# Performance work log

Hardware: AMD Instinct MI355X
Metric: run time of the kernel (lower is better)

The kernel has to match this reference:

```python
import jax, jax.numpy as jnp
import numpy as np

N_NODES = 100000
LN_EPS = 1e-5
NEG_SLOPE = 0.2


def setup_inputs() -> dict:
    key = jax.random.key(0)
    ks = jax.random.split(key, 6)
    N, E, NIN, EDIM, NOUT, H = N_NODES, 1600000, 64, 32, 128, 4
    x = jax.random.normal(ks[0], (N, NIN), dtype=jnp.float32)
    edge_index = jax.random.randint(ks[1], (2, E), 0, N, dtype=jnp.int64)
    edge_attr = jax.random.normal(ks[2], (E, EDIM), dtype=jnp.float32)
    # xavier-uniform linear weights (torch layout: [out, in])
    def xavier(k, fan_out, fan_in):
        lim = float(np.sqrt(6.0 / (fan_in + fan_out)))
        return jax.random.uniform(k, (fan_out, fan_in), jnp.float32, -lim, lim)
    W_msg = xavier(ks[3], NOUT, NIN + EDIM)          # (128, 96)
    W_att = xavier(ks[4], H, 2 * NIN + EDIM)         # (4, 160)
    bias = jnp.zeros((NOUT,), jnp.float32)
    ln_gamma = jnp.ones((NOUT,), jnp.float32)
    ln_beta = jnp.zeros((NOUT,), jnp.float32)
    return {"x": x, "edge_index": edge_index, "edge_attr": edge_attr,
            "W_msg": W_msg, "W_att": W_att, "bias": bias,
            "ln_gamma": ln_gamma, "ln_beta": ln_beta}


def reference(x, edge_index, edge_attr, W_msg, W_att, bias, ln_gamma, ln_beta):
    N = x.shape[0]
    H = W_att.shape[0]
    src, dst = edge_index[0], edge_index[1]
    xs = x[src]                                       # (E, node_in) gather
    xd = x[dst]                                       # (E, node_in) gather
    # message: W_msg @ [h_u ; x_uv]
    msg_in = jnp.concatenate([xs, edge_attr], axis=-1)            # (E, 96)
    msgs = msg_in @ W_msg.T                                        # (E, out_dim)
    msgs = msgs.reshape(-1, H, W_msg.shape[0] // H)                # (E, H, D)
    # attention logits: LeakyReLU(W_att @ [h_u ; h_v ; x_uv])
    att_in = jnp.concatenate([xs, xd, edge_attr], axis=-1)         # (E, 160)
    logits = att_in @ W_att.T                                      # (E, H)
    logits = jax.nn.leaky_relu(logits, NEG_SLOPE)
    # per-destination-node sparse softmax
    seg_max = jax.ops.segment_max(logits, dst, num_segments=N)     # (N, H)
    exp_l = jnp.exp(logits - seg_max[dst])                         # (E, H)
    seg_sum = jax.ops.segment_sum(exp_l, dst, num_segments=N)      # (N, H)
    att = exp_l / (seg_sum[dst] + 1e-9)                            # (E, H)
    # weighted scatter-add aggregation
    weighted = msgs * att[..., None]                               # (E, H, D)
    out = jax.ops.segment_sum(weighted, dst, num_segments=N)       # (N, H, D)
    out = out.reshape(N, -1) + bias                                # concat heads
    # layer norm over feature dim
    mu = out.mean(axis=-1, keepdims=True)
    var = out.var(axis=-1, keepdims=True)
    out = (out - mu) * jax.lax.rsqrt(var + LN_EPS) * ln_gamma + ln_beta
    return out
```

## Files before the change

kernel.cpp:

```cpp
#include <hip/hip_runtime.h>
#include <hip/hip_bf16.h>

typedef __attribute__((ext_vector_type(8))) short short8;
typedef __attribute__((ext_vector_type(4))) float f32x4;

__device__ __forceinline__ unsigned short fbf(float f) {
  union { float f; unsigned u; } v; v.f = f;
  unsigned r = v.u + 0x7fffu + ((v.u >> 16) & 1u);
  return (unsigned short)(r >> 16);
}
__device__ __forceinline__ unsigned pk2(float a, float b) {
  return (unsigned)fbf(a) | ((unsigned)fbf(b) << 16);
}
__device__ __forceinline__ float ubf(unsigned hi) {
  union { unsigned u; float f; } v; v.u = hi << 16; return v.f;
}
__device__ __forceinline__ float dot4(float4 a, float4 b) {
  return fmaf(a.x, b.x, fmaf(a.y, b.y, fmaf(a.z, b.z, a.w * b.w)));
}

__global__ void k_count(const int* __restrict__ dst, int E, int* __restrict__ deg) {
  for (int i = blockIdx.x * blockDim.x + threadIdx.x; i < E; i += gridDim.x * blockDim.x)
    atomicAdd(&deg[dst[i]], 1);
}

__global__ void k_scan1(const int* __restrict__ deg, int N, int* __restrict__ part,
                        int* __restrict__ bsum) {
  __shared__ int tmp[1024];
  int tid = threadIdx.x;
  int i = blockIdx.x * 1024 + tid;
  int v = (i < N) ? deg[i] : 0;
  tmp[tid] = v;
  __syncthreads();
  for (int ofs = 1; ofs < 1024; ofs <<= 1) {
    int t = (tid >= ofs) ? tmp[tid - ofs] : 0;
    __syncthreads();
    tmp[tid] += t;
    __syncthreads();
  }
  if (i < N) part[i] = tmp[tid] - v;
  if (tid == 1023) bsum[blockIdx.x] = tmp[tid];
}

__global__ void k_scan2(int* __restrict__ part, const int* __restrict__ bsum, int N,
                        int* __restrict__ cursor) {
  __shared__ int sbase;
  if (threadIdx.x == 0) {
    int b = 0;
    for (int j = 0; j < (int)blockIdx.x; j++) b += bsum[j];
    sbase = b;
  }
  __syncthreads();
  int i = blockIdx.x * 1024 + threadIdx.x;
  if (i < N) {
    int o = part[i] + sbase;
    part[i] = o;
    cursor[i] = o;
  }
}

__global__ void k_fill(const int* __restrict__ src, const int* __restrict__ dst, int E,
                       int* __restrict__ cursor, int2* __restrict__ csr2) {
  for (int i = blockIdx.x * blockDim.x + threadIdx.x; i < E; i += gridDim.x * blockDim.x) {
    int d = dst[i];
    int slot = atomicAdd(&cursor[d], 1);
    csr2[slot] = make_int2(src[i], i);
  }
}

__launch_bounds__(256)
__global__ void k_pre(const float* __restrict__ x, const float* __restrict__ W_att,
                      float4* __restrict__ A_s, float4* __restrict__ A_d, int N) {
  __shared__ float4 s_wa[160];
  if (threadIdx.x < 160) s_wa[threadIdx.x] = ((const float4*)W_att)[threadIdx.x];
  __syncthreads();
  for (int v = blockIdx.x * blockDim.x + threadIdx.x; v < N; v += gridDim.x * blockDim.x) {
    const float4* xp = (const float4*)&x[v * 64];
    float4 xq[16];
    #pragma unroll
    for (int k = 0; k < 16; k++) xq[k] = xp[k];
    float as[4] = {}, ad[4] = {};
    #pragma unroll
    for (int h = 0; h < 4; h++) {
      #pragma unroll
      for (int k = 0; k < 16; k++) {
        as[h] += dot4(s_wa[h * 40 + k], xq[k]);
        ad[h] += dot4(s_wa[h * 40 + 16 + k], xq[k]);
      }
    }
    A_s[v] = make_float4(as[0], as[1], as[2], as[3]);
    A_d[v] = make_float4(ad[0], ad[1], ad[2], ad[3]);
  }
}

__launch_bounds__(256)
__global__ void k_cvt(const float* __restrict__ x, unsigned* __restrict__ xb2, int n4) {
  for (int i = blockIdx.x * blockDim.x + threadIdx.x; i < n4; i += gridDim.x * blockDim.x) {
    float4 t = ((const float4*)x)[i];
    xb2[i * 2]     = pk2(t.x, t.y);
    xb2[i * 2 + 1] = pk2(t.z, t.w);
  }
}

__launch_bounds__(256)
__global__ void k_agg(const unsigned short* __restrict__ xb, const float* __restrict__ ea,
                      const float4* __restrict__ A_s, const float4* __restrict__ A_d,
                      const float* __restrict__ W_att,
                      const int2* __restrict__ csr2, const int* __restrict__ offsets,
                      const int* __restrict__ deg,
                      unsigned short* __restrict__ agg, float* __restrict__ denom, int N) {
  __shared__ int2 s_ids[4][8];
  __shared__ float4 s_att[4][8];
  const int lane = threadIdx.x & 63;
  const int wvb = threadIdx.x >> 6;
  const int wv = (blockIdx.x * blockDim.x + threadIdx.x) >> 6;
  const int nw = (gridDim.x * blockDim.x) >> 6;
  const int l8 = lane & 7;
  const int l32 = lane & 31;
  const bool hi = (lane & 32) != 0;
  const int pj = lane >> 3;
  const int jc = lane & 7;

  float4 wea[4];
  #pragma unroll
  for (int h = 0; h < 4; h++)
    wea[h] = *(const float4*)&W_att[h * 160 + 128 + jc * 4];

  for (int v = wv; v < N; v += nw) {
    const int start = offsets[v];
    const int dg = deg[v];
    const float4 adv = A_d[v];
    float ax0 = 0, ax1 = 0, ax2 = 0, ax3 = 0, ae0 = 0, ae1 = 0;
    float ss0 = 0, ss1 = 0, ss2 = 0, ss3 = 0;

    if (dg > 0) {
      const int ng = (dg + 7) >> 3;
      int2 cur = csr2[start + min(l8, dg - 1)];
      for (int g = 0; g < ng; g++) {
        if (lane < 8) s_ids[wvb][lane] = cur;
        if (g + 1 < ng)
          cur = csr2[start + min((g + 1) * 8 + l8, dg - 1)];
        int2 idl = s_ids[wvb][pj];
        float4 ef = *(const float4*)&ea[(size_t)idl.y * 32 + jc * 4];
        float4 asv = A_s[idl.x];
        int sp[8], ep[8];
        #pragma unroll
        for (int p = 0; p < 8; p++) { int2 t = s_ids[wvb][p]; sp[p] = t.x; ep[p] = t.y; }
        float xv[8], ev[8];
        #pragma unroll
        for (int p = 0; p < 8; p++) xv[p] = ubf(xb[(size_t)sp[p] * 64 + lane]);
        #pragma unroll
        for (int p = 0; p < 8; p++) ev[p] = ea[(size_t)ep[p] * 32 + l32];
        float lp0 = dot4(wea[0], ef), lp1 = dot4(wea[1], ef);
        float lp2 = dot4(wea[2], ef), lp3 = dot4(wea[3], ef);
        #pragma unroll
        for (int m = 1; m <= 4; m <<= 1) {
          lp0 += __shfl_xor(lp0, m, 64);
          lp1 += __shfl_xor(lp1, m, 64);
          lp2 += __shfl_xor(lp2, m, 64);
          lp3 += __shfl_xor(lp3, m, 64);
        }
        const float msk = (g * 8 + pj < dg) ? 1.f : 0.f;
        float4 av; float lg;
        lg = lp0 + asv.x + adv.x; lg = (lg > 0.f) ? lg : 0.2f * lg; av.x = msk * __expf(lg);
        lg = lp1 + asv.y + adv.y; lg = (lg > 0.f) ? lg : 0.2f * lg; av.y = msk * __expf(lg);
        lg = lp2 + asv.z + adv.z; lg = (lg > 0.f) ? lg : 0.2f * lg; av.z = msk * __expf(lg);
        lg = lp3 + asv.w + adv.w; lg = (lg > 0.f) ? lg : 0.2f * lg; av.w = msk * __expf(lg);
        if (jc == 0) s_att[wvb][pj] = av;
        #pragma unroll
        for (int p = 0; p < 8; p++) {
          float4 ap = s_att[wvb][p];
          ax0 = fmaf(ap.x, xv[p], ax0);
          ax1 = fmaf(ap.y, xv[p], ax1);
          ax2 = fmaf(ap.z, xv[p], ax2);
          ax3 = fmaf(ap.w, xv[p], ax3);
          ae0 = fmaf(hi ? ap.z : ap.x, ev[p], ae0);
          ae1 = fmaf(hi ? ap.w : ap.y, ev[p], ae1);
          ss0 += ap.x; ss1 += ap.y; ss2 += ap.z; ss3 += ap.w;
        }
      }
    }
    const int base = v * 384;
    agg[base + lane]       = fbf(ax0);
    agg[base + 96 + lane]  = fbf(ax1);
    agg[base + 192 + lane] = fbf(ax2);
    agg[base + 288 + lane] = fbf(ax3);
    const int hA = hi ? 2 : 0;
    agg[base + hA * 96 + 64 + l32]       = fbf(ae0);
    agg[base + (hA + 1) * 96 + 64 + l32] = fbf(ae1);
    if (lane == 0) ((float4*)denom)[v] = make_float4(ss0, ss1, ss2, ss3);
  }
}

__launch_bounds__(128)
__global__ void k_out(const unsigned short* __restrict__ agg, const float* __restrict__ W_msg,
                      const float* __restrict__ denom, const float* __restrict__ bias,
                      const float* __restrict__ gamma, const float* __restrict__ beta,
                      float* __restrict__ out, int N, int T) {
  __shared__ float s_den[64];
  __shared__ float s_sum[2][16], s_sq[2][16];
  const int f = threadIdx.x;
  const int w = f >> 6;
  const int l = f & 63;
  const int c16 = l & 15;
  const int rg = l >> 4;

  short8 wb[2][2][3];
  float biasv[2][2], gv[2][2], bv[2][2];
  #pragma unroll
  for (int hh = 0; hh < 2; hh++) {
    const int head = 2 * w + hh;
    #pragma unroll
    for (int ct = 0; ct < 2; ct++) {
      const int q = head * 32 + ct * 16 + c16;
      biasv[hh][ct] = bias[q]; gv[hh][ct] = gamma[q]; bv[hh][ct] = beta[q];
      #pragma unroll
      for (int kk = 0; kk < 3; kk++) {
        const float* p = &W_msg[q * 96 + kk * 32 + rg * 8];
        short8 s;
        #pragma unroll
        for (int i = 0; i < 8; i++) s[i] = (short)fbf(p[i]);
        wb[hh][ct][kk] = s;
      }
    }
  }

  for (int t = blockIdx.x; t < T; t += gridDim.x) {
    const int n0 = t * 16;
    if (f < 64) s_den[f] = denom[min(n0 + (f >> 2), N - 1) * 4 + (f & 3)];
    __syncthreads();

    f32x4 c[2][2] = {{{0.f,0.f,0.f,0.f},{0.f,0.f,0.f,0.f}},
                     {{0.f,0.f,0.f,0.f},{0.f,0.f,0.f,0.f}}};
    const int nA = min(n0 + c16, N - 1);
    #pragma unroll
    for (int hh = 0; hh < 2; hh++) {
      const int head = 2 * w + hh;
      #pragma unroll
      for (int kk = 0; kk < 3; kk++) {
        short8 a = *(const short8*)&agg[nA * 384 + head * 96 + kk * 32 + rg * 8];
        c[hh][0] = __builtin_amdgcn_mfma_f32_16x16x32_bf16(a, wb[hh][0][kk], c[hh][0], 0, 0, 0);
        c[hh][1] = __builtin_amdgcn_mfma_f32_16x16x32_bf16(a, wb[hh][1][kk], c[hh][1], 0, 0, 0);
      }
    }

    float val[2][2][4];
    #pragma unroll
    for (int hh = 0; hh < 2; hh++)
      #pragma unroll
      for (int ct = 0; ct < 2; ct++)
        #pragma unroll
        for (int r = 0; r < 4; r++) {
          const float d = s_den[(rg * 4 + r) * 4 + (2 * w + hh)] + 1e-9f;
          val[hh][ct][r] = c[hh][ct][r] / d + biasv[hh][ct];
        }

    float sr[4], qr[4];
    #pragma unroll
    for (int r = 0; r < 4; r++) {
      float s = 0.f, q2 = 0.f;
      #pragma unroll
      for (int hh = 0; hh < 2; hh++)
        #pragma unroll
        for (int ct = 0; ct < 2; ct++) { s += val[hh][ct][r]; q2 = fmaf(val[hh][ct][r], val[hh][ct][r], q2); }
      #pragma unroll
      for (int m = 1; m <= 8; m <<= 1) { s += __shfl_xor(s, m, 64); q2 += __shfl_xor(q2, m, 64); }
      sr[r] = s; qr[r] = q2;
    }
    if (c16 == 0) {
      #pragma unroll
      for (int r = 0; r < 4; r++) { s_sum[w][rg * 4 + r] = sr[r]; s_sq[w][rg * 4 + r] = qr[r]; }
    }
    __syncthreads();

    float mean[4], rstd[4];
    #pragma unroll
    for (int r = 0; r < 4; r++) {
      const int ni = rg * 4 + r;
      mean[r] = (s_sum[0][ni] + s_sum[1][ni]) * (1.f / 128.f);
      const float m2 = (s_sq[0][ni] + s_sq[1][ni]) * (1.f / 128.f);
      rstd[r] = rsqrtf(m2 - mean[r] * mean[r] + 1e-5f);
    }
    #pragma unroll
    for (int hh = 0; hh < 2; hh++)
      #pragma unroll
      for (int ct = 0; ct < 2; ct++)
        #pragma unroll
        for (int r = 0; r < 4; r++) {
          const int n = n0 + rg * 4 + r;
          if (n < N)
            out[n * 128 + (2 * w + hh) * 32 + ct * 16 + c16] =
                (val[hh][ct][r] - mean[r]) * rstd[r] * gv[hh][ct] + bv[hh][ct];
        }
    __syncthreads();
  }
}

extern "C" void kernel_launch(void* const* d_in, const int* in_sizes, int n_in,
                              void* d_out, int out_size, void* d_ws, size_t ws_size,
                              hipStream_t stream) {
  const float* x     = (const float*)d_in[0];
  const int*   ei    = (const int*)d_in[1];
  const float* ea    = (const float*)d_in[2];
  const float* W_msg = (const float*)d_in[3];
  const float* W_att = (const float*)d_in[4];
  const float* bias  = (const float*)d_in[5];
  const float* gamma = (const float*)d_in[6];
  const float* beta  = (const float*)d_in[7];
  float* out = (float*)d_out;

  const int N = in_sizes[0] / 64;
  const int E = in_sizes[1] / 2;
  const int* esrc = ei;
  const int* edst = ei + E;

  char* p = (char*)d_ws;
  int* deg      = (int*)p;            p += (size_t)N * 4;
  int* offsets  = (int*)p;            p += (size_t)N * 4;
  int* cursor   = (int*)p;            p += (size_t)N * 4;
  int* bsum     = (int*)p;            p += 2048 * 4;
  int2* csr2    = (int2*)p;           p += (size_t)E * 8;
  float4* A_s   = (float4*)p;         p += (size_t)N * 16;
  float4* A_d   = (float4*)p;         p += (size_t)N * 16;
  unsigned short* xb = (unsigned short*)p; p += (size_t)N * 64 * 2;
  unsigned short* agg = (unsigned short*)p; p += (size_t)N * 384 * 2;
  float* denom  = (float*)p;

  hipMemsetAsync(deg, 0, (size_t)N * sizeof(int), stream);
  const int SB = (N + 1023) / 1024;
  const int T = (N + 15) / 16;

  k_count<<<2048, 256, 0, stream>>>(edst, E, deg);
  k_scan1<<<SB, 1024, 0, stream>>>(deg, N, offsets, bsum);
  k_scan2<<<SB, 1024, 0, stream>>>(offsets, bsum, N, cursor);
  k_fill<<<2048, 256, 0, stream>>>(esrc, edst, E, cursor, csr2);
  k_pre<<<(N + 255) / 256, 256, 0, stream>>>(x, W_att, A_s, A_d, N);
  k_cvt<<<2048, 256, 0, stream>>>(x, (unsigned*)xb, N * 16);
  k_agg<<<2048, 256, 0, stream>>>(xb, ea, A_s, A_d, W_att, csr2, offsets, deg,
                                  agg, denom, N);
  k_out<<<2048, 128, 0, stream>>>(agg, W_msg, denom, bias, gamma, beta, out, N, T);
}
```

Baseline: 413.9 us.

## Software-pipeline edge gathers in aggregation kernel and fuse bf16 conversion into prep

```diff
diff --git a/kernel.cpp b/kernel.cpp
--- a/kernel.cpp
+++ b/kernel.cpp
@@ -69,8 +69,9 @@
 }
 
 __launch_bounds__(256)
-__global__ void k_pre(const float* __restrict__ x, const float* __restrict__ W_att,
-                      float4* __restrict__ A_s, float4* __restrict__ A_d, int N) {
+__global__ void k_prep(const float* __restrict__ x, const float* __restrict__ W_att,
+                       float4* __restrict__ A_s, float4* __restrict__ A_d,
+                       unsigned* __restrict__ xb32, int N) {
   __shared__ float4 s_wa[160];
   if (threadIdx.x < 160) s_wa[threadIdx.x] = ((const float4*)W_att)[threadIdx.x];
   __syncthreads();
@@ -90,95 +91,161 @@
     }
     A_s[v] = make_float4(as[0], as[1], as[2], as[3]);
     A_d[v] = make_float4(ad[0], ad[1], ad[2], ad[3]);
-  }
-}
-
-__launch_bounds__(256)
-__global__ void k_cvt(const float* __restrict__ x, unsigned* __restrict__ xb2, int n4) {
-  for (int i = blockIdx.x * blockDim.x + threadIdx.x; i < n4; i += gridDim.x * blockDim.x) {
-    float4 t = ((const float4*)x)[i];
-    xb2[i * 2]     = pk2(t.x, t.y);
-    xb2[i * 2 + 1] = pk2(t.z, t.w);
-  }
-}
-
-__launch_bounds__(256)
+    #pragma unroll
+    for (int k = 0; k < 16; k++) {
+      xb32[v * 32 + 2 * k]     = pk2(xq[k].x, xq[k].y);
+      xb32[v * 32 + 2 * k + 1] = pk2(xq[k].z, xq[k].w);
+    }
+  }
+}
+
+struct GBuf {
+  unsigned short xv[8];
+  float ev[8];
+  float4 ef, asv;
+};
+
+__launch_bounds__(256, 4)
 __global__ void k_agg(const unsigned short* __restrict__ xb, const float* __restrict__ ea,
                       const float4* __restrict__ A_s, const float4* __restrict__ A_d,
-                      const float* __restrict__ W_att,
                       const int2* __restrict__ csr2, const int* __restrict__ offsets,
-                      const int* __restrict__ deg,
-                      unsigned short* __restrict__ agg, float* __restrict__ denom, int N) {
-  __shared__ int2 s_ids[4][8];
+                      const int* __restrict__ deg, const float* __restrict__ W_att,
+                      unsigned short* __restrict__ agg, float* __restrict__ denom,
+                      int N, int Ec) {
+  __shared__ int2 s_ids[4][32];
   __shared__ float4 s_att[4][8];
   const int lane = threadIdx.x & 63;
   const int wvb = threadIdx.x >> 6;
   const int wv = (blockIdx.x * blockDim.x + threadIdx.x) >> 6;
   const int nw = (gridDim.x * blockDim.x) >> 6;
-  const int l8 = lane & 7;
   const int l32 = lane & 31;
   const bool hi = (lane & 32) != 0;
   const int pj = lane >> 3;
   const int jc = lane & 7;
-
-  float4 wea[4];
-  #pragma unroll
-  for (int h = 0; h < 4; h++)
-    wea[h] = *(const float4*)&W_att[h * 160 + 128 + jc * 4];
-
-  for (int v = wv; v < N; v += nw) {
-    const int start = offsets[v];
-    const int dg = deg[v];
-    const float4 adv = A_d[v];
+  const float jc0f = (jc == 0) ? 1.f : 0.f;
+
+  const float4 wea0 = *(const float4*)&W_att[0 * 160 + 128 + jc * 4];
+  const float4 wea1 = *(const float4*)&W_att[1 * 160 + 128 + jc * 4];
+  const float4 wea2 = *(const float4*)&W_att[2 * 160 + 128 + jc * 4];
+  const float4 wea3 = *(const float4*)&W_att[3 * 160 + 128 + jc * 4];
+
+#define ISSUE_G(B, g) do {                                                  \
+    const int qo8_ = ((g) & 3) * 8;                                         \
+    _Pragma("unroll")                                                       \
+    for (int p = 0; p < 8; p++) {                                           \
+      int2 idp = s_ids[wvb][qo8_ + p];                                      \
+      int sps = __builtin_amdgcn_readfirstlane(idp.x);                      \
+      int eps = __builtin_amdgcn_readfirstlane(idp.y);                      \
+      B.xv[p] = xb[(size_t)sps * 64 + lane];                                \
+      B.ev[p] = ea[(size_t)eps * 32 + l32];                                 \
+    }                                                                       \
+    int2 idl_ = s_ids[wvb][qo8_ + pj];                                      \
+    B.ef = *(const float4*)&ea[(size_t)idl_.y * 32 + jc * 4];               \
+    B.asv = A_s[idl_.x];                                                    \
+  } while (0)
+
+#define COMPUTE_G(B, g) do {                                                \
+    float lp0 = dot4(wea0, B.ef), lp1 = dot4(wea1, B.ef);                   \
+    float lp2 = dot4(wea2, B.ef), lp3 = dot4(wea3, B.ef);                   \
+    _Pragma("unroll")                                                       \
+    for (int m = 1; m <= 4; m <<= 1) {                                      \
+      lp0 += __shfl_xor(lp0, m, 64); lp1 += __shfl_xor(lp1, m, 64);         \
+      lp2 += __shfl_xor(lp2, m, 64); lp3 += __shfl_xor(lp3, m, 64);         \
+    }                                                                       \
+    const float msk_ = ((g) * 8 + pj < dg) ? 1.f : 0.f;                     \
+    float4 av_; float lg_;                                                  \
+    lg_ = lp0 + B.asv.x + adv.x; lg_ = (lg_ > 0.f) ? lg_ : 0.2f * lg_;      \
+    av_.x = msk_ * __expf(lg_);                                             \
+    lg_ = lp1 + B.asv.y + adv.y; lg_ = (lg_ > 0.f) ? lg_ : 0.2f * lg_;      \
+    av_.y = msk_ * __expf(lg_);                                             \
+    lg_ = lp2 + B.asv.z + adv.z; lg_ = (lg_ > 0.f) ? lg_ : 0.2f * lg_;      \
+    av_.z = msk_ * __expf(lg_);                                             \
+    lg_ = lp3 + B.asv.w + adv.w; lg_ = (lg_ > 0.f) ? lg_ : 0.2f * lg_;      \
+    av_.w = msk_ * __expf(lg_);                                             \
+    if (jc == 0) s_att[wvb][pj] = av_;                                      \
+    ssa.x = fmaf(av_.x, jc0f, ssa.x); ssa.y = fmaf(av_.y, jc0f, ssa.y);     \
+    ssa.z = fmaf(av_.z, jc0f, ssa.z); ssa.w = fmaf(av_.w, jc0f, ssa.w);     \
+    _Pragma("unroll")                                                       \
+    for (int p = 0; p < 8; p++) {                                           \
+      float4 ap = s_att[wvb][p];                                            \
+      float xf = ubf((unsigned)B.xv[p]);                                    \
+      ax0 = fmaf(ap.x, xf, ax0); ax1 = fmaf(ap.y, xf, ax1);                 \
+      ax2 = fmaf(ap.z, xf, ax2); ax3 = fmaf(ap.w, xf, ax3);                 \
+      ae0 = fmaf(hi ? ap.z : ap.x, B.ev[p], ae0);                           \
+      ae1 = fmaf(hi ? ap.w : ap.y, B.ev[p], ae1);                           \
+    }                                                                       \
+  } while (0)
+
+  int v = wv;
+  int start = 0, dg = 0;
+  float4 adv = make_float4(0.f, 0.f, 0.f, 0.f);
+  int2 qcur = make_int2(0, 0);
+  if (v < N) {
+    start = offsets[v];
+    dg = deg[v];
+    adv = A_d[v];
+    int lim = start + ((dg > 0) ? min(l32, dg - 1) : 0);
+    qcur = csr2[min(lim, Ec - 1)];
+  }
+
+  while (v < N) {
+    const int v_next = v + nw;
+    int start_n = 0, dg_n = 0;
+    float4 adv_n = make_float4(0.f, 0.f, 0.f, 0.f);
+    if (v_next < N) {
+      start_n = offsets[v_next];
+      dg_n = deg[v_next];
+      adv_n = A_d[v_next];
+    }
+
     float ax0 = 0, ax1 = 0, ax2 = 0, ax3 = 0, ae0 = 0, ae1 = 0;
-    float ss0 = 0, ss1 = 0, ss2 = 0, ss3 = 0;
+    float4 ssa = make_float4(0.f, 0.f, 0.f, 0.f);
+    int2 qn = make_int2(0, 0);
+    bool qn_done = false;
 
     if (dg > 0) {
+      if (lane < 32) s_ids[wvb][l32] = qcur;
       const int ng = (dg + 7) >> 3;
-      int2 cur = csr2[start + min(l8, dg - 1)];
-      for (int g = 0; g < ng; g++) {
-        if (lane < 8) s_ids[wvb][lane] = cur;
-        if (g + 1 < ng)
-          cur = csr2[start + min((g + 1) * 8 + l8, dg - 1)];
-        int2 idl = s_ids[wvb][pj];
-        float4 ef = *(const float4*)&ea[(size_t)idl.y * 32 + jc * 4];
-        float4 asv = A_s[idl.x];
-        int sp[8], ep[8];
-        #pragma unroll
-        for (int p = 0; p < 8; p++) { int2 t = s_ids[wvb][p]; sp[p] = t.x; ep[p] = t.y; }
-        float xv[8], ev[8];
-        #pragma unroll
-        for (int p = 0; p < 8; p++) xv[p] = ubf(xb[(size_t)sp[p] * 64 + lane]);
-        #pragma unroll
-        for (int p = 0; p < 8; p++) ev[p] = ea[(size_t)ep[p] * 32 + l32];
-        float lp0 = dot4(wea[0], ef), lp1 = dot4(wea[1], ef);
-        float lp2 = dot4(wea[2], ef), lp3 = dot4(wea[3], ef);
-        #pragma unroll
-        for (int m = 1; m <= 4; m <<= 1) {
-          lp0 += __shfl_xor(lp0, m, 64);
-          lp1 += __shfl_xor(lp1, m, 64);
-          lp2 += __shfl_xor(lp2, m, 64);
-          lp3 += __shfl_xor(lp3, m, 64);
+      GBuf A, B;
+      ISSUE_G(A, 0);
+      int g = 0;
+      while (true) {
+        if (g + 1 < ng) {
+          if (((g + 1) & 3) == 0) {
+            int2 q = csr2[start + min((g + 1) * 8 + l32, dg - 1)];
+            if (lane < 32) s_ids[wvb][l32] = q;
+          }
+          ISSUE_G(B, g + 1);
         }
-        const float msk = (g * 8 + pj < dg) ? 1.f : 0.f;
-        float4 av; float lg;
-        lg = lp0 + asv.x + adv.x; lg = (lg > 0.f) ? lg : 0.2f * lg; av.x = msk * __expf(lg);
-        lg = lp1 + asv.y + adv.y; lg = (lg > 0.f) ? lg : 0.2f * lg; av.y = msk * __expf(lg);
-        lg = lp2 + asv.z + adv.z; lg = (lg > 0.f) ? lg : 0.2f * lg; av.z = msk * __expf(lg);
-        lg = lp3 + asv.w + adv.w; lg = (lg > 0.f) ? lg : 0.2f * lg; av.w = msk * __expf(lg);
-        if (jc == 0) s_att[wvb][pj] = av;
-        #pragma unroll
-        for (int p = 0; p < 8; p++) {
-          float4 ap = s_att[wvb][p];
-          ax0 = fmaf(ap.x, xv[p], ax0);
-          ax1 = fmaf(ap.y, xv[p], ax1);
-          ax2 = fmaf(ap.z, xv[p], ax2);
-          ax3 = fmaf(ap.w, xv[p], ax3);
-          ae0 = fmaf(hi ? ap.z : ap.x, ev[p], ae0);
-          ae1 = fmaf(hi ? ap.w : ap.y, ev[p], ae1);
-          ss0 += ap.x; ss1 += ap.y; ss2 += ap.z; ss3 += ap.w;
+        COMPUTE_G(A, g);
+        if (g == 0 && v_next < N) {
+          int lim = start_n + ((dg_n > 0) ? min(l32, dg_n - 1) : 0);
+          qn = csr2[min(lim, Ec - 1)];
+          qn_done = true;
         }
+        if (++g >= ng) break;
+        if (g + 1 < ng) {
+          if (((g + 1) & 3) == 0) {
+            int2 q = csr2[start + min((g + 1) * 8 + l32, dg - 1)];
+            if (lane < 32) s_ids[wvb][l32] = q;
+          }
+          ISSUE_G(A, g + 1);
+        }
+        COMPUTE_G(B, g);
+        if (++g >= ng) break;
       }
+    }
+    if (!qn_done && v_next < N) {
+      int lim = start_n + ((dg_n > 0) ? min(l32, dg_n - 1) : 0);
+      qn = csr2[min(lim, Ec - 1)];
+    }
+
+    #pragma unroll
+    for (int m = 1; m <= 32; m <<= 1) {
+      ssa.x += __shfl_xor(ssa.x, m, 64);
+      ssa.y += __shfl_xor(ssa.y, m, 64);
+      ssa.z += __shfl_xor(ssa.z, m, 64);
+      ssa.w += __shfl_xor(ssa.w, m, 64);
     }
     const int base = v * 384;
     agg[base + lane]       = fbf(ax0);
@@ -188,8 +255,12 @@
     const int hA = hi ? 2 : 0;
     agg[base + hA * 96 + 64 + l32]       = fbf(ae0);
     agg[base + (hA + 1) * 96 + 64 + l32] = fbf(ae1);
-    if (lane == 0) ((float4*)denom)[v] = make_float4(ss0, ss1, ss2, ss3);
-  }
+    if (lane == 0) ((float4*)denom)[v] = ssa;
+
+    v = v_next; start = start_n; dg = dg_n; adv = adv_n; qcur = qn;
+  }
+#undef ISSUE_G
+#undef COMPUTE_G
 }
 
 __launch_bounds__(128)
@@ -334,9 +405,8 @@
   k_scan1<<<SB, 1024, 0, stream>>>(deg, N, offsets, bsum);
   k_scan2<<<SB, 1024, 0, stream>>>(offsets, bsum, N, cursor);
   k_fill<<<2048, 256, 0, stream>>>(esrc, edst, E, cursor, csr2);
-  k_pre<<<(N + 255) / 256, 256, 0, stream>>>(x, W_att, A_s, A_d, N);
-  k_cvt<<<2048, 256, 0, stream>>>(x, (unsigned*)xb, N * 16);
-  k_agg<<<2048, 256, 0, stream>>>(xb, ea, A_s, A_d, W_att, csr2, offsets, deg,
-                                  agg, denom, N);
+  k_prep<<<(N + 255) / 256, 256, 0, stream>>>(x, W_att, A_s, A_d, (unsigned*)xb, N);
+  k_agg<<<2048, 256, 0, stream>>>(xb, ea, A_s, A_d, csr2, offsets, deg, W_att,
+                                  agg, denom, N, E);
   k_out<<<2048, 128, 0, stream>>>(agg, W_msg, denom, bias, gamma, beta, out, N, T);
 }
```

After: 919.6 us. 122% more time.
